# Kernel tuning notes

Hardware: AMD Instinct MI355X
Metric: run time of the kernel (lower is better)

Reference implementation:

```python
import jax, jax.numpy as jnp
import numpy as np

N_NODES = 100000
N_EDGES = 1000000
D = 128
NEG_SLOPE = 0.01  # F.leaky_relu default


def setup_inputs() -> dict:
    key = jax.random.key(0)
    k1, k2, k3, k4, k5, k6 = jax.random.split(key, 6)
    h_src = jax.random.normal(k1, (N_NODES, D), dtype=jnp.float32)
    h_dst = jax.random.normal(k2, (N_NODES, D), dtype=jnp.float32)
    edge_src = jax.random.randint(k3, (N_EDGES,), 0, N_NODES, dtype=jnp.int32)
    edge_dst = jax.random.randint(k4, (N_EDGES,), 0, N_NODES, dtype=jnp.int32)
    # xavier_normal_ on a (1, D) tensor -> std = sqrt(2/(1+D))
    std = float(np.sqrt(2.0 / (1.0 + D)))
    attn_l = jax.random.normal(k5, (D,), dtype=jnp.float32) * std
    attn_r = jax.random.normal(k6, (D,), dtype=jnp.float32) * std
    bias = jnp.zeros((D,), dtype=jnp.float32)
    return {"h_src": h_src, "h_dst": h_dst, "edge_src": edge_src,
            "edge_dst": edge_dst, "attn_l": attn_l, "attn_r": attn_r,
            "bias": bias}


def reference(h_src, h_dst, edge_src, edge_dst, attn_l, attn_r, bias):
    # Per-node attention projections (dot with attn vectors): [N]
    el = h_src @ attn_l
    er = h_dst @ attn_r
    # Edge scores: gather + add + leaky_relu, [E]
    e = jax.nn.leaky_relu(el[edge_src] + er[edge_dst], negative_slope=NEG_SLOPE)
    # Segment (per-destination) softmax over incoming edges
    m = jax.ops.segment_max(e, edge_dst, num_segments=N_NODES)  # [N]
    a = jnp.exp(e - m[edge_dst])                                # [E]
    s = jax.ops.segment_sum(a, edge_dst, num_segments=N_NODES)  # [N]
    alpha = a / s[edge_dst]                                     # [E]
    # dropout p=0.0 -> identity
    # Weighted message + scatter-sum aggregation: [N, D]
    msg = h_src[edge_src] * alpha[:, None]                      # [E, D]
    h_N = jax.ops.segment_sum(msg, edge_dst, num_segments=N_NODES)
    return h_N + bias
```

## Files before the change

### kernel.cpp

```cpp
#include <hip/hip_runtime.h>
#include <math.h>

#define N_NODES 100000
#define N_EDGES 1000000
#define D 128
#define NEG_SLOPE 0.01f
#define SCAN_BLOCK 1024
#define N_SCAN_BLOCKS ((N_NODES + SCAN_BLOCK - 1) / SCAN_BLOCK)

__device__ __forceinline__ unsigned int f2bf(float f) {
    unsigned int u = __float_as_uint(f);
    return (u + 0x7FFFu + ((u >> 16) & 1u)) >> 16;
}

__global__ void node_proj_cvt_kernel(const float* __restrict__ h_src,
                                     const float* __restrict__ h_dst,
                                     const float* __restrict__ attn_l,
                                     const float* __restrict__ attn_r,
                                     float* __restrict__ el,
                                     float* __restrict__ er,
                                     unsigned int* __restrict__ hbf,
                                     int* __restrict__ cnt,
                                     unsigned long long* __restrict__ st) {
    int t = blockIdx.x * blockDim.x + threadIdx.x;
    if (t < N_NODES) cnt[t] = 0;
    if (t < N_SCAN_BLOCKS) st[t] = 0ULL;
    int node = t >> 6;
    int lane = threadIdx.x & 63;
    if (node >= N_NODES) return;
    float2 vs = ((const float2*)(h_src + (size_t)node * D))[lane];
    float2 vd = ((const float2*)(h_dst + (size_t)node * D))[lane];
    float2 wl = ((const float2*)attn_l)[lane];
    float2 wr = ((const float2*)attn_r)[lane];
    hbf[(size_t)node * 64 + lane] = f2bf(vs.x) | (f2bf(vs.y) << 16);
    float sl = vs.x * wl.x + vs.y * wl.y;
    float sr = vd.x * wr.x + vd.y * wr.y;
    #pragma unroll
    for (int off = 32; off > 0; off >>= 1) {
        sl += __shfl_down(sl, off, 64);
        sr += __shfl_down(sr, off, 64);
    }
    if (lane == 0) { el[node] = sl; er[node] = sr; }
}

__global__ void edge_w_slot_kernel(const int* __restrict__ esrc,
                                   const int* __restrict__ edst,
                                   const float* __restrict__ el,
                                   const float* __restrict__ er,
                                   float* __restrict__ w,
                                   int* __restrict__ slot,
                                   int* __restrict__ cnt) {
    int i = blockIdx.x * blockDim.x + threadIdx.x;
    if (i >= N_EDGES) return;
    int s = esrc[i], d = edst[i];
    float v = el[s] + er[d];
    v = (v > 0.0f) ? v : NEG_SLOPE * v;
    w[i] = __expf(v);
    slot[i] = atomicAdd(&cnt[d], 1);
}

__global__ void scan_kernel(const int* __restrict__ cnt,
                            int* __restrict__ row_start,
                            unsigned long long* __restrict__ st) {
    __shared__ int buf[2][SCAN_BLOCK];
    __shared__ int s_running;
    int tid = threadIdx.x;
    int gid = blockIdx.x * SCAN_BLOCK + tid;
    int x = (gid < N_NODES) ? cnt[gid] : 0;
    int pi = 0;
    buf[0][tid] = x;
    __syncthreads();
    for (int off = 1; off < SCAN_BLOCK; off <<= 1) {
        int v = buf[pi][tid];
        if (tid >= off) v += buf[pi][tid - off];
        buf[1 - pi][tid] = v;
        pi = 1 - pi;
        __syncthreads();
    }
    int incl = buf[pi][tid];
    int total = buf[pi][SCAN_BLOCK - 1];
    if (tid == 0) {
        if (blockIdx.x == 0) {
            __hip_atomic_store(&st[0], (2ULL << 32) | (unsigned int)total,
                               __ATOMIC_RELEASE, __HIP_MEMORY_SCOPE_AGENT);
            s_running = 0;
        } else {
            __hip_atomic_store(&st[blockIdx.x], (1ULL << 32) | (unsigned int)total,
                               __ATOMIC_RELEASE, __HIP_MEMORY_SCOPE_AGENT);
            int running = 0;
            int j = blockIdx.x - 1;
            for (;;) {
                unsigned long long s;
                do {
                    s = __hip_atomic_load(&st[j], __ATOMIC_ACQUIRE,
                                          __HIP_MEMORY_SCOPE_AGENT);
                } while ((s >> 32) == 0);
                running += (int)(unsigned int)s;
                if ((s >> 32) == 2) break;
                --j;
            }
            __hip_atomic_store(&st[blockIdx.x],
                               (2ULL << 32) | (unsigned int)(running + total),
                               __ATOMIC_RELEASE, __HIP_MEMORY_SCOPE_AGENT);
            s_running = running;
        }
    }
    __syncthreads();
    int running = s_running;
    if (gid < N_NODES) row_start[gid + 1] = running + incl;
    if (gid == 0) row_start[0] = 0;
}

__global__ void fill_kernel(const int* __restrict__ esrc,
                            const int* __restrict__ edst,
                            const int* __restrict__ slot,
                            const float* __restrict__ w,
                            const int* __restrict__ row_start,
                            int2* __restrict__ csr) {
    int i = blockIdx.x * blockDim.x + threadIdx.x;
    if (i >= N_EDGES) return;
    int d = edst[i];
    int2 p;
    p.x = esrc[i];
    p.y = __float_as_int(w[i]);
    csr[row_start[d] + slot[i]] = p;
}

__global__ void aggregate_kernel(const unsigned int* __restrict__ hbf,
                                 const int* __restrict__ row_start,
                                 const int2* __restrict__ csr,
                                 const float* __restrict__ bias,
                                 float* __restrict__ out) {
    int t = blockIdx.x * blockDim.x + threadIdx.x;
    int node = t >> 6;
    if (node >= N_NODES) return;
    int lane = threadIdx.x & 63;
    int q = lane >> 4, ql = lane & 15;
    int start = row_start[node];
    int deg = row_start[node + 1] - start;
    float4 b0 = ((const float4*)bias)[ql * 2];
    float4 b1 = ((const float4*)bias)[ql * 2 + 1];
    float4* op = (float4*)(out + (size_t)node * D);
    if (deg == 0) {
        if (q == 0) { op[ql * 2] = b0; op[ql * 2 + 1] = b1; }
        return;
    }
    float acc[8] = {0, 0, 0, 0, 0, 0, 0, 0};
    float sum = 0.0f;
    for (int base = 0; base < deg; base += 4) {
        int e = base + q;
        int2 p = csr[start + min(e, deg - 1)];
        float wk = (e < deg) ? __int_as_float(p.y) : 0.0f;
        uint4 g = ((const uint4*)(hbf + (size_t)p.x * 64))[ql];
        acc[0] += wk * __uint_as_float(g.x << 16);
        acc[1] += wk * __uint_as_float(g.x & 0xFFFF0000u);
        acc[2] += wk * __uint_as_float(g.y << 16);
        acc[3] += wk * __uint_as_float(g.y & 0xFFFF0000u);
        acc[4] += wk * __uint_as_float(g.z << 16);
        acc[5] += wk * __uint_as_float(g.z & 0xFFFF0000u);
        acc[6] += wk * __uint_as_float(g.w << 16);
        acc[7] += wk * __uint_as_float(g.w & 0xFFFF0000u);
        sum += wk;
    }
    #pragma unroll
    for (int off = 16; off <= 32; off <<= 1) {
        sum += __shfl_xor(sum, off, 64);
        #pragma unroll
        for (int i = 0; i < 8; ++i) acc[i] += __shfl_xor(acc[i], off, 64);
    }
    if (q == 0) {
        float inv = 1.0f / sum;
        float4 o0 = { acc[0] * inv + b0.x, acc[1] * inv + b0.y,
                      acc[2] * inv + b0.z, acc[3] * inv + b0.w };
        float4 o1 = { acc[4] * inv + b1.x, acc[5] * inv + b1.y,
                      acc[6] * inv + b1.z, acc[7] * inv + b1.w };
        op[ql * 2]     = o0;
        op[ql * 2 + 1] = o1;
    }
}

extern "C" void kernel_launch(void* const* d_in, const int* in_sizes, int n_in,
                              void* d_out, int out_size, void* d_ws, size_t ws_size,
                              hipStream_t stream) {
    const float* h_src  = (const float*)d_in[0];
    const float* h_dst  = (const float*)d_in[1];
    const int*   esrc   = (const int*)d_in[2];
    const int*   edst   = (const int*)d_in[3];
    const float* attn_l = (const float*)d_in[4];
    const float* attn_r = (const float*)d_in[5];
    const float* bias   = (const float*)d_in[6];
    float* out = (float*)d_out;

    int2*               csr       = (int2*)d_ws;
    unsigned int*       hbf       = (unsigned int*)(csr + N_EDGES);
    unsigned long long* st        = (unsigned long long*)(hbf + (size_t)N_NODES * 64);
    float*              el        = (float*)(st + 128);
    float*              er        = el + N_NODES;
    int*                cnt       = (int*)(er + N_NODES);
    int*                row_start = cnt + N_NODES;
    float*              w         = (float*)(row_start + N_NODES + 2);
    int*                slot      = (int*)(w + N_EDGES);

    node_proj_cvt_kernel<<<(N_NODES + 3) / 4, 256, 0, stream>>>(
        h_src, h_dst, attn_l, attn_r, el, er, hbf, cnt, st);

    edge_w_slot_kernel<<<(N_EDGES + 255) / 256, 256, 0, stream>>>(
        esrc, edst, el, er, w, slot, cnt);

    scan_kernel<<<N_SCAN_BLOCKS, SCAN_BLOCK, 0, stream>>>(cnt, row_start, st);

    fill_kernel<<<(N_EDGES + 255) / 256, 256, 0, stream>>>(
        esrc, edst, slot, w, row_start, csr);

    aggregate_kernel<<<(N_NODES + 3) / 4, 256, 0, stream>>>(
        hbf, row_start, csr, bias, out);
}
```

Before: 276.1 us.

## Fuse GAT pipeline into one cooperative persistent kernel with grid syncs

Replaces the five separate launches (projection, edge weights, scan, CSR fill, aggregation) with a single cooperatively launched persistent kernel. The phases are separated by grid-wide barriers, and the scan becomes a two-level block scan with a single-block pass over block sums. Slot and weight are packed into one int2 so the fill phase reads one array instead of two. This is meant to remove launch gaps and the decoupled look-back scan. The cost is six grid syncs and a fixed grid of 1024x256 threads, which may give the gather-heavy aggregation fewer resident waves than before.

After: 944.8 us. 242% more time.

```diff
diff --git a/kernel.cpp b/kernel.cpp
--- a/kernel.cpp
+++ b/kernel.cpp
@@ -1,181 +1,163 @@
 #include <hip/hip_runtime.h>
+#include <hip/hip_cooperative_groups.h>
 #include <math.h>
+
+namespace cg = cooperative_groups;
 
 #define N_NODES 100000
 #define N_EDGES 1000000
 #define D 128
 #define NEG_SLOPE 0.01f
-#define SCAN_BLOCK 1024
-#define N_SCAN_BLOCKS ((N_NODES + SCAN_BLOCK - 1) / SCAN_BLOCK)
+#define GRID_BLOCKS 1024
+#define BLOCK 256
+#define NTHREADS (GRID_BLOCKS * BLOCK)
+#define NWAVES (NTHREADS / 64)
+#define SCAN_BLOCKS ((N_NODES + BLOCK - 1) / BLOCK)
 
 __device__ __forceinline__ unsigned int f2bf(float f) {
     unsigned int u = __float_as_uint(f);
     return (u + 0x7FFFu + ((u >> 16) & 1u)) >> 16;
 }
 
-__global__ void node_proj_cvt_kernel(const float* __restrict__ h_src,
-                                     const float* __restrict__ h_dst,
-                                     const float* __restrict__ attn_l,
-                                     const float* __restrict__ attn_r,
-                                     float* __restrict__ el,
-                                     float* __restrict__ er,
-                                     unsigned int* __restrict__ hbf,
-                                     int* __restrict__ cnt,
-                                     unsigned long long* __restrict__ st) {
-    int t = blockIdx.x * blockDim.x + threadIdx.x;
-    if (t < N_NODES) cnt[t] = 0;
-    if (t < N_SCAN_BLOCKS) st[t] = 0ULL;
-    int node = t >> 6;
-    int lane = threadIdx.x & 63;
-    if (node >= N_NODES) return;
-    float2 vs = ((const float2*)(h_src + (size_t)node * D))[lane];
-    float2 vd = ((const float2*)(h_dst + (size_t)node * D))[lane];
-    float2 wl = ((const float2*)attn_l)[lane];
-    float2 wr = ((const float2*)attn_r)[lane];
-    hbf[(size_t)node * 64 + lane] = f2bf(vs.x) | (f2bf(vs.y) << 16);
-    float sl = vs.x * wl.x + vs.y * wl.y;
-    float sr = vd.x * wr.x + vd.y * wr.y;
-    #pragma unroll
-    for (int off = 32; off > 0; off >>= 1) {
-        sl += __shfl_down(sl, off, 64);
-        sr += __shfl_down(sr, off, 64);
-    }
-    if (lane == 0) { el[node] = sl; er[node] = sr; }
-}
+__global__ __launch_bounds__(BLOCK, 4) void mega_kernel(
+    const float* __restrict__ h_src, const float* __restrict__ h_dst,
+    const int* __restrict__ esrc, const int* __restrict__ edst,
+    const float* __restrict__ attn_l, const float* __restrict__ attn_r,
+    const float* __restrict__ bias, float* __restrict__ out,
+    unsigned int* __restrict__ hbf, float* __restrict__ el,
+    float* __restrict__ er, int* __restrict__ cnt,
+    int* __restrict__ row_start, int* __restrict__ blocksum,
+    int2* __restrict__ sw, int2* __restrict__ csr)
+{
+    cg::grid_group grid = cg::this_grid();
+    __shared__ int sbuf[2][512];
+    const int tid  = blockIdx.x * BLOCK + threadIdx.x;
+    const int lane = threadIdx.x & 63;
+    const int gwave = tid >> 6;
 
-__global__ void edge_w_slot_kernel(const int* __restrict__ esrc,
-                                   const int* __restrict__ edst,
-                                   const float* __restrict__ el,
-                                   const float* __restrict__ er,
-                                   float* __restrict__ w,
-                                   int* __restrict__ slot,
-                                   int* __restrict__ cnt) {
-    int i = blockIdx.x * blockDim.x + threadIdx.x;
-    if (i >= N_EDGES) return;
-    int s = esrc[i], d = edst[i];
-    float v = el[s] + er[d];
-    v = (v > 0.0f) ? v : NEG_SLOPE * v;
-    w[i] = __expf(v);
-    slot[i] = atomicAdd(&cnt[d], 1);
-}
-
-__global__ void scan_kernel(const int* __restrict__ cnt,
-                            int* __restrict__ row_start,
-                            unsigned long long* __restrict__ st) {
-    __shared__ int buf[2][SCAN_BLOCK];
-    __shared__ int s_running;
-    int tid = threadIdx.x;
-    int gid = blockIdx.x * SCAN_BLOCK + tid;
-    int x = (gid < N_NODES) ? cnt[gid] : 0;
-    int pi = 0;
-    buf[0][tid] = x;
-    __syncthreads();
-    for (int off = 1; off < SCAN_BLOCK; off <<= 1) {
-        int v = buf[pi][tid];
-        if (tid >= off) v += buf[pi][tid - off];
-        buf[1 - pi][tid] = v;
-        pi = 1 - pi;
-        __syncthreads();
-    }
-    int incl = buf[pi][tid];
-    int total = buf[pi][SCAN_BLOCK - 1];
-    if (tid == 0) {
-        if (blockIdx.x == 0) {
-            __hip_atomic_store(&st[0], (2ULL << 32) | (unsigned int)total,
-                               __ATOMIC_RELEASE, __HIP_MEMORY_SCOPE_AGENT);
-            s_running = 0;
-        } else {
-            __hip_atomic_store(&st[blockIdx.x], (1ULL << 32) | (unsigned int)total,
-                               __ATOMIC_RELEASE, __HIP_MEMORY_SCOPE_AGENT);
-            int running = 0;
-            int j = blockIdx.x - 1;
-            for (;;) {
-                unsigned long long s;
-                do {
-                    s = __hip_atomic_load(&st[j], __ATOMIC_ACQUIRE,
-                                          __HIP_MEMORY_SCOPE_AGENT);
-                } while ((s >> 32) == 0);
-                running += (int)(unsigned int)s;
-                if ((s >> 32) == 2) break;
-                --j;
+    for (int t = tid; t < N_NODES; t += NTHREADS) cnt[t] = 0;
+    {
+        float2 wl = ((const float2*)attn_l)[lane];
+        float2 wr = ((const float2*)attn_r)[lane];
+        for (int node = gwave; node < N_NODES; node += NWAVES) {
+            float2 vs = ((const float2*)(h_src + (size_t)node * D))[lane];
+            float2 vd = ((const float2*)(h_dst + (size_t)node * D))[lane];
+            hbf[(size_t)node * 64 + lane] = f2bf(vs.x) | (f2bf(vs.y) << 16);
+            float sl = vs.x * wl.x + vs.y * wl.y;
+            float sr = vd.x * wr.x + vd.y * wr.y;
+            #pragma unroll
+            for (int off = 32; off > 0; off >>= 1) {
+                sl += __shfl_down(sl, off, 64);
+                sr += __shfl_down(sr, off, 64);
             }
-            __hip_atomic_store(&st[blockIdx.x],
-                               (2ULL << 32) | (unsigned int)(running + total),
-                               __ATOMIC_RELEASE, __HIP_MEMORY_SCOPE_AGENT);
-            s_running = running;
+            if (lane == 0) { el[node] = sl; er[node] = sr; }
         }
     }
-    __syncthreads();
-    int running = s_running;
-    if (gid < N_NODES) row_start[gid + 1] = running + incl;
-    if (gid == 0) row_start[0] = 0;
-}
+    grid.sync();
 
-__global__ void fill_kernel(const int* __restrict__ esrc,
-                            const int* __restrict__ edst,
-                            const int* __restrict__ slot,
-                            const float* __restrict__ w,
-                            const int* __restrict__ row_start,
-                            int2* __restrict__ csr) {
-    int i = blockIdx.x * blockDim.x + threadIdx.x;
-    if (i >= N_EDGES) return;
-    int d = edst[i];
-    int2 p;
-    p.x = esrc[i];
-    p.y = __float_as_int(w[i]);
-    csr[row_start[d] + slot[i]] = p;
-}
+    for (int i = tid; i < N_EDGES; i += NTHREADS) {
+        int s = esrc[i], d = edst[i];
+        float v = el[s] + er[d];
+        v = (v > 0.0f) ? v : NEG_SLOPE * v;
+        int sl_ = atomicAdd(&cnt[d], 1);
+        sw[i] = make_int2(sl_, __float_as_int(__expf(v)));
+    }
+    grid.sync();
 
-__global__ void aggregate_kernel(const unsigned int* __restrict__ hbf,
-                                 const int* __restrict__ row_start,
-                                 const int2* __restrict__ csr,
-                                 const float* __restrict__ bias,
-                                 float* __restrict__ out) {
-    int t = blockIdx.x * blockDim.x + threadIdx.x;
-    int node = t >> 6;
-    if (node >= N_NODES) return;
-    int lane = threadIdx.x & 63;
-    int q = lane >> 4, ql = lane & 15;
-    int start = row_start[node];
-    int deg = row_start[node + 1] - start;
-    float4 b0 = ((const float4*)bias)[ql * 2];
-    float4 b1 = ((const float4*)bias)[ql * 2 + 1];
-    float4* op = (float4*)(out + (size_t)node * D);
-    if (deg == 0) {
-        if (q == 0) { op[ql * 2] = b0; op[ql * 2 + 1] = b1; }
-        return;
+    int incl = 0;
+    {
+        int x = (tid < N_NODES) ? cnt[tid] : 0;
+        int pi = 0;
+        sbuf[0][threadIdx.x] = x;
+        __syncthreads();
+        for (int off = 1; off < BLOCK; off <<= 1) {
+            int v = sbuf[pi][threadIdx.x];
+            if ((int)threadIdx.x >= off) v += sbuf[pi][threadIdx.x - off];
+            sbuf[1 - pi][threadIdx.x] = v;
+            pi ^= 1;
+            __syncthreads();
+        }
+        incl = sbuf[pi][threadIdx.x];
+        if (threadIdx.x == BLOCK - 1 && blockIdx.x < SCAN_BLOCKS)
+            blocksum[blockIdx.x] = incl;
     }
-    float acc[8] = {0, 0, 0, 0, 0, 0, 0, 0};
-    float sum = 0.0f;
-    for (int base = 0; base < deg; base += 4) {
-        int e = base + q;
-        int2 p = csr[start + min(e, deg - 1)];
-        float wk = (e < deg) ? __int_as_float(p.y) : 0.0f;
-        uint4 g = ((const uint4*)(hbf + (size_t)p.x * 64))[ql];
-        acc[0] += wk * __uint_as_float(g.x << 16);
-        acc[1] += wk * __uint_as_float(g.x & 0xFFFF0000u);
-        acc[2] += wk * __uint_as_float(g.y << 16);
-        acc[3] += wk * __uint_as_float(g.y & 0xFFFF0000u);
-        acc[4] += wk * __uint_as_float(g.z << 16);
-        acc[5] += wk * __uint_as_float(g.z & 0xFFFF0000u);
-        acc[6] += wk * __uint_as_float(g.w << 16);
-        acc[7] += wk * __uint_as_float(g.w & 0xFFFF0000u);
-        sum += wk;
+    grid.sync();
+
+    if (blockIdx.x == 0) {
+        int i0 = threadIdx.x, i1 = threadIdx.x + 256;
+        int a0 = (i0 < SCAN_BLOCKS) ? blocksum[i0] : 0;
+        int a1 = (i1 < SCAN_BLOCKS) ? blocksum[i1] : 0;
+        sbuf[0][i0] = a0; sbuf[0][i1] = a1;
+        __syncthreads();
+        int pi = 0;
+        for (int off = 1; off < 512; off <<= 1) {
+            int v0 = sbuf[pi][i0]; if (i0 >= off) v0 += sbuf[pi][i0 - off];
+            int v1 = sbuf[pi][i1]; if (i1 >= off) v1 += sbuf[pi][i1 - off];
+            sbuf[1 - pi][i0] = v0; sbuf[1 - pi][i1] = v1;
+            pi ^= 1;
+            __syncthreads();
+        }
+        if (i0 < SCAN_BLOCKS) blocksum[i0] = sbuf[pi][i0] - a0;
+        if (i1 < SCAN_BLOCKS) blocksum[i1] = sbuf[pi][i1] - a1;
     }
-    #pragma unroll
-    for (int off = 16; off <= 32; off <<= 1) {
-        sum += __shfl_xor(sum, off, 64);
-        #pragma unroll
-        for (int i = 0; i < 8; ++i) acc[i] += __shfl_xor(acc[i], off, 64);
+    grid.sync();
+
+    if (tid < N_NODES) row_start[tid + 1] = incl + blocksum[blockIdx.x];
+    if (tid == 0) row_start[0] = 0;
+    grid.sync();
+
+    for (int i = tid; i < N_EDGES; i += NTHREADS) {
+        int d = edst[i];
+        int2 p = sw[i];
+        csr[row_start[d] + p.x] = make_int2(esrc[i], p.y);
     }
-    if (q == 0) {
-        float inv = 1.0f / sum;
-        float4 o0 = { acc[0] * inv + b0.x, acc[1] * inv + b0.y,
-                      acc[2] * inv + b0.z, acc[3] * inv + b0.w };
-        float4 o1 = { acc[4] * inv + b1.x, acc[5] * inv + b1.y,
-                      acc[6] * inv + b1.z, acc[7] * inv + b1.w };
-        op[ql * 2]     = o0;
-        op[ql * 2 + 1] = o1;
+    grid.sync();
+
+    {
+        int q = lane >> 4, ql = lane & 15;
+        float4 b0 = ((const float4*)bias)[ql * 2];
+        float4 b1 = ((const float4*)bias)[ql * 2 + 1];
+        for (int node = gwave; node < N_NODES; node += NWAVES) {
+            int start = row_start[node];
+            int deg = row_start[node + 1] - start;
+            float4* op = (float4*)(out + (size_t)node * D);
+            if (deg == 0) {
+                if (q == 0) { op[ql * 2] = b0; op[ql * 2 + 1] = b1; }
+                continue;
+            }
+            float acc[8] = {0, 0, 0, 0, 0, 0, 0, 0};
+            float sum = 0.0f;
+            for (int base = 0; base < deg; base += 4) {
+                int e = base + q;
+                int2 p = csr[start + min(e, deg - 1)];
+                float wk = (e < deg) ? __int_as_float(p.y) : 0.0f;
+                uint4 g = ((const uint4*)(hbf + (size_t)p.x * 64))[ql];
+                acc[0] += wk * __uint_as_float(g.x << 16);
+                acc[1] += wk * __uint_as_float(g.x & 0xFFFF0000u);
+                acc[2] += wk * __uint_as_float(g.y << 16);
+                acc[3] += wk * __uint_as_float(g.y & 0xFFFF0000u);
+                acc[4] += wk * __uint_as_float(g.z << 16);
+                acc[5] += wk * __uint_as_float(g.z & 0xFFFF0000u);
+                acc[6] += wk * __uint_as_float(g.w << 16);
+                acc[7] += wk * __uint_as_float(g.w & 0xFFFF0000u);
+                sum += wk;
+            }
+            #pragma unroll
+            for (int off = 16; off <= 32; off <<= 1) {
+                sum += __shfl_xor(sum, off, 64);
+                #pragma unroll
+                for (int i = 0; i < 8; ++i) acc[i] += __shfl_xor(acc[i], off, 64);
+            }
+            if (q == 0) {
+                float inv = 1.0f / sum;
+                float4 o0 = { acc[0] * inv + b0.x, acc[1] * inv + b0.y,
+                              acc[2] * inv + b0.z, acc[3] * inv + b0.w };
+                float4 o1 = { acc[4] * inv + b1.x, acc[5] * inv + b1.y,
+                              acc[6] * inv + b1.z, acc[7] * inv + b1.w };
+                op[ql * 2]     = o0;
+                op[ql * 2 + 1] = o1;
+            }
+        }
     }
 }
 
@@ -191,27 +173,21 @@
     const float* bias   = (const float*)d_in[6];
     float* out = (float*)d_out;
 
-    int2*               csr       = (int2*)d_ws;
-    unsigned int*       hbf       = (unsigned int*)(csr + N_EDGES);
-    unsigned long long* st        = (unsigned long long*)(hbf + (size_t)N_NODES * 64);
-    float*              el        = (float*)(st + 128);
-    float*              er        = el + N_NODES;
-    int*                cnt       = (int*)(er + N_NODES);
-    int*                row_start = cnt + N_NODES;
-    float*              w         = (float*)(row_start + N_NODES + 2);
-    int*                slot      = (int*)(w + N_EDGES);
+    int2*         csr       = (int2*)d_ws;
+    unsigned int* hbf       = (unsigned int*)(csr + N_EDGES);
+    int2*         sw        = (int2*)(hbf + (size_t)N_NODES * 64);
+    float*        el        = (float*)(sw + N_EDGES);
+    float*        er        = el + N_NODES;
+    int*          cnt       = (int*)(er + N_NODES);
+    int*          row_start = cnt + N_NODES;
+    int*          blocksum  = row_start + N_NODES + 2;
 
-    node_proj_cvt_kernel<<<(N_NODES + 3) / 4, 256, 0, stream>>>(
-        h_src, h_dst, attn_l, attn_r, el, er, hbf, cnt, st);
-
-    edge_w_slot_kernel<<<(N_EDGES + 255) / 256, 256, 0, stream>>>(
-        esrc, edst, el, er, w, slot, cnt);
-
-    scan_kernel<<<N_SCAN_BLOCKS, SCAN_BLOCK, 0, stream>>>(cnt, row_start, st);
-
-    fill_kernel<<<(N_EDGES + 255) / 256, 256, 0, stream>>>(
-        esrc, edst, slot, w, row_start, csr);
-
-    aggregate_kernel<<<(N_NODES + 3) / 4, 256, 0, stream>>>(
-        hbf, row_start, csr, bias, out);
+    void* args[] = {
+        (void*)&h_src, (void*)&h_dst, (void*)&esrc, (void*)&edst,
+        (void*)&attn_l, (void*)&attn_r, (void*)&bias, (void*)&out,
+        (void*)&hbf, (void*)&el, (void*)&er, (void*)&cnt,
+        (void*)&row_start, (void*)&blocksum, (void*)&sw, (void*)&csr
+    };
+    hipLaunchCooperativeKernel((void*)mega_kernel, dim3(GRID_BLOCKS),
+                               dim3(BLOCK), args, 0, stream);
 }
```

## Fuse degree histogram into projection kernel and compute edge weights in fill

Applied to the files above, without the earlier changes.

Folds the per-destination degree histogram into the node projection kernel and drops the separate edge-weight/slot kernel. The fill kernel now computes the leaky-relu exp weight and takes its position from an atomic cursor seeded by the scan with exclusive offsets. This removes the w and slot intermediate arrays and one launch. The aggregate kernel also loads 64 CSR entries per wave at once and broadcasts them with shuffles instead of each quarter-wave reloading them. The costs are a memset launch and atomic contention moving into the fill pass.

Result: slower. 301.3 us (+9.1%).

```diff
diff --git a/kernel.cpp b/kernel.cpp
--- a/kernel.cpp
+++ b/kernel.cpp
@@ -13,19 +13,18 @@
     return (u + 0x7FFFu + ((u >> 16) & 1u)) >> 16;
 }
 
-__global__ void node_proj_cvt_kernel(const float* __restrict__ h_src,
-                                     const float* __restrict__ h_dst,
-                                     const float* __restrict__ attn_l,
-                                     const float* __restrict__ attn_r,
-                                     float* __restrict__ el,
-                                     float* __restrict__ er,
-                                     unsigned int* __restrict__ hbf,
-                                     int* __restrict__ cnt,
-                                     unsigned long long* __restrict__ st) {
-    int t = blockIdx.x * blockDim.x + threadIdx.x;
-    if (t < N_NODES) cnt[t] = 0;
-    if (t < N_SCAN_BLOCKS) st[t] = 0ULL;
-    int node = t >> 6;
+__global__ void proj_hist_kernel(const float* __restrict__ h_src,
+                                 const float* __restrict__ h_dst,
+                                 const float* __restrict__ attn_l,
+                                 const float* __restrict__ attn_r,
+                                 const int* __restrict__ edst,
+                                 float* __restrict__ el,
+                                 float* __restrict__ er,
+                                 unsigned int* __restrict__ hbf,
+                                 int* __restrict__ cnt) {
+    int tid = blockIdx.x * blockDim.x + threadIdx.x;
+    if (tid < N_EDGES) atomicAdd(&cnt[edst[tid]], 1);
+    int node = tid >> 6;
     int lane = threadIdx.x & 63;
     if (node >= N_NODES) return;
     float2 vs = ((const float2*)(h_src + (size_t)node * D))[lane];
@@ -43,24 +42,9 @@
     if (lane == 0) { el[node] = sl; er[node] = sr; }
 }
 
-__global__ void edge_w_slot_kernel(const int* __restrict__ esrc,
-                                   const int* __restrict__ edst,
-                                   const float* __restrict__ el,
-                                   const float* __restrict__ er,
-                                   float* __restrict__ w,
-                                   int* __restrict__ slot,
-                                   int* __restrict__ cnt) {
-    int i = blockIdx.x * blockDim.x + threadIdx.x;
-    if (i >= N_EDGES) return;
-    int s = esrc[i], d = edst[i];
-    float v = el[s] + er[d];
-    v = (v > 0.0f) ? v : NEG_SLOPE * v;
-    w[i] = __expf(v);
-    slot[i] = atomicAdd(&cnt[d], 1);
-}
-
 __global__ void scan_kernel(const int* __restrict__ cnt,
                             int* __restrict__ row_start,
+                            int* __restrict__ cursor,
                             unsigned long long* __restrict__ st) {
     __shared__ int buf[2][SCAN_BLOCK];
     __shared__ int s_running;
@@ -74,7 +58,7 @@
         int v = buf[pi][tid];
         if (tid >= off) v += buf[pi][tid - off];
         buf[1 - pi][tid] = v;
-        pi = 1 - pi;
+        pi ^= 1;
         __syncthreads();
     }
     int incl = buf[pi][tid];
@@ -107,23 +91,27 @@
     }
     __syncthreads();
     int running = s_running;
-    if (gid < N_NODES) row_start[gid + 1] = running + incl;
+    if (gid < N_NODES) {
+        int excl = running + incl - x;
+        row_start[gid + 1] = running + incl;
+        cursor[gid] = excl;
+    }
     if (gid == 0) row_start[0] = 0;
 }
 
 __global__ void fill_kernel(const int* __restrict__ esrc,
                             const int* __restrict__ edst,
-                            const int* __restrict__ slot,
-                            const float* __restrict__ w,
-                            const int* __restrict__ row_start,
+                            const float* __restrict__ el,
+                            const float* __restrict__ er,
+                            int* __restrict__ cursor,
                             int2* __restrict__ csr) {
     int i = blockIdx.x * blockDim.x + threadIdx.x;
     if (i >= N_EDGES) return;
-    int d = edst[i];
-    int2 p;
-    p.x = esrc[i];
-    p.y = __float_as_int(w[i]);
-    csr[row_start[d] + slot[i]] = p;
+    int s = esrc[i], d = edst[i];
+    float v = el[s] + er[d];
+    v = (v > 0.0f) ? v : NEG_SLOPE * v;
+    int pos = atomicAdd(&cursor[d], 1);
+    csr[pos] = make_int2(s, __float_as_int(__expf(v)));
 }
 
 __global__ void aggregate_kernel(const unsigned int* __restrict__ hbf,
@@ -147,20 +135,25 @@
     }
     float acc[8] = {0, 0, 0, 0, 0, 0, 0, 0};
     float sum = 0.0f;
-    for (int base = 0; base < deg; base += 4) {
-        int e = base + q;
-        int2 p = csr[start + min(e, deg - 1)];
-        float wk = (e < deg) ? __int_as_float(p.y) : 0.0f;
-        uint4 g = ((const uint4*)(hbf + (size_t)p.x * 64))[ql];
-        acc[0] += wk * __uint_as_float(g.x << 16);
-        acc[1] += wk * __uint_as_float(g.x & 0xFFFF0000u);
-        acc[2] += wk * __uint_as_float(g.y << 16);
-        acc[3] += wk * __uint_as_float(g.y & 0xFFFF0000u);
-        acc[4] += wk * __uint_as_float(g.z << 16);
-        acc[5] += wk * __uint_as_float(g.z & 0xFFFF0000u);
-        acc[6] += wk * __uint_as_float(g.w << 16);
-        acc[7] += wk * __uint_as_float(g.w & 0xFFFF0000u);
-        sum += wk;
+    for (int cbase = 0; cbase < deg; cbase += 64) {
+        int nchunk = min(64, deg - cbase);
+        int2 p = csr[start + cbase + min(lane, nchunk - 1)];
+        for (int base = 0; base < nchunk; base += 4) {
+            int e = base + q;
+            int   sk = __shfl(p.x, e, 64);
+            int   wb = __shfl(p.y, e, 64);
+            float wk = (e < nchunk) ? __int_as_float(wb) : 0.0f;
+            uint4 g = ((const uint4*)(hbf + (size_t)sk * 64))[ql];
+            acc[0] += wk * __uint_as_float(g.x << 16);
+            acc[1] += wk * __uint_as_float(g.x & 0xFFFF0000u);
+            acc[2] += wk * __uint_as_float(g.y << 16);
+            acc[3] += wk * __uint_as_float(g.y & 0xFFFF0000u);
+            acc[4] += wk * __uint_as_float(g.z << 16);
+            acc[5] += wk * __uint_as_float(g.z & 0xFFFF0000u);
+            acc[6] += wk * __uint_as_float(g.w << 16);
+            acc[7] += wk * __uint_as_float(g.w & 0xFFFF0000u);
+            sum += wk;
+        }
     }
     #pragma unroll
     for (int off = 16; off <= 32; off <<= 1) {
@@ -193,24 +186,23 @@
 
     int2*               csr       = (int2*)d_ws;
     unsigned int*       hbf       = (unsigned int*)(csr + N_EDGES);
-    unsigned long long* st        = (unsigned long long*)(hbf + (size_t)N_NODES * 64);
-    float*              el        = (float*)(st + 128);
+    float*              el        = (float*)(hbf + (size_t)N_NODES * 64);
     float*              er        = el + N_NODES;
     int*                cnt       = (int*)(er + N_NODES);
-    int*                row_start = cnt + N_NODES;
-    float*              w         = (float*)(row_start + N_NODES + 2);
-    int*                slot      = (int*)(w + N_EDGES);
-
-    node_proj_cvt_kernel<<<(N_NODES + 3) / 4, 256, 0, stream>>>(
-        h_src, h_dst, attn_l, attn_r, el, er, hbf, cnt, st);
-
-    edge_w_slot_kernel<<<(N_EDGES + 255) / 256, 256, 0, stream>>>(
-        esrc, edst, el, er, w, slot, cnt);
-
-    scan_kernel<<<N_SCAN_BLOCKS, SCAN_BLOCK, 0, stream>>>(cnt, row_start, st);
+    unsigned long long* st        = (unsigned long long*)(cnt + N_NODES);
+    int*                row_start = (int*)(st + 128);
+    int*                cursor    = row_start + N_NODES + 2;
+
+    hipMemsetAsync(cnt, 0, N_NODES * sizeof(int) + 128 * sizeof(unsigned long long),
+                   stream);
+
+    proj_hist_kernel<<<(N_NODES + 3) / 4, 256, 0, stream>>>(
+        h_src, h_dst, attn_l, attn_r, edst, el, er, hbf, cnt);
+
+    scan_kernel<<<N_SCAN_BLOCKS, SCAN_BLOCK, 0, stream>>>(cnt, row_start, cursor, st);
 
     fill_kernel<<<(N_EDGES + 255) / 256, 256, 0, stream>>>(
-        esrc, edst, slot, w, row_start, csr);
+        esrc, edst, el, er, cursor, csr);
 
     aggregate_kernel<<<(N_NODES + 3) / 4, 256, 0, stream>>>(
         hbf, row_start, csr, bias, out);
```
